# Performance work log

Hardware: AMD Instinct MI355X
Metric: run time of the kernel (lower is better)

The kernel has to match this reference:

```python
import jax, jax.numpy as jnp
import numpy as np

B, T = 32, 2048
HID, ACT, SRC, AGE = 512, 64, 2, 16
TRUNK, BINS, PHASES = 256, 20, 7
IN_DIM = HID + ACT + SRC + AGE  # 594


def setup_inputs() -> dict:
    key = jax.random.key(0)
    ks = jax.random.split(key, 16)
    s_in = 1.0 / np.sqrt(IN_DIM)
    s_tr = 1.0 / np.sqrt(TRUNK)
    s_h = 1.0 / np.sqrt(HID)
    return {
        "h_t": jax.random.normal(ks[0], (B, T, HID), jnp.float32),
        "a_t": jax.random.normal(ks[1], (B, T, ACT), jnp.float32),
        "d_t": jax.random.normal(ks[2], (B, T, SRC), jnp.float32),
        "age_embed": jax.random.normal(ks[3], (B, T, AGE), jnp.float32),
        "trunk_w": jax.random.normal(ks[4], (IN_DIM, TRUNK), jnp.float32) * s_in,
        "trunk_b": jax.random.normal(ks[5], (TRUNK,), jnp.float32) * s_in,
        "inst_base_w": jax.random.normal(ks[6], (TRUNK, BINS), jnp.float32) * s_tr,
        "inst_base_b": jax.random.normal(ks[7], (BINS,), jnp.float32) * s_tr,
        "group_base_w": jax.random.normal(ks[8], (TRUNK, BINS), jnp.float32) * s_tr,
        "group_base_b": jax.random.normal(ks[9], (BINS,), jnp.float32) * s_tr,
        "inst_exp_w": jax.random.normal(ks[10], (PHASES, TRUNK, BINS), jnp.float32) * s_tr,
        "inst_exp_b": jax.random.normal(ks[11], (PHASES, BINS), jnp.float32) * s_tr,
        "group_exp_w": jax.random.normal(ks[12], (PHASES, TRUNK, BINS), jnp.float32) * s_tr,
        "group_exp_b": jax.random.normal(ks[13], (PHASES, BINS), jnp.float32) * s_tr,
        "router_w": jax.random.normal(ks[14], (HID, PHASES), jnp.float32) * s_h,
        "router_b": jax.random.normal(ks[15], (PHASES,), jnp.float32) * s_h,
    }


def reference(h_t, a_t, d_t, age_embed,
              trunk_w, trunk_b, inst_base_w, inst_base_b,
              group_base_w, group_base_b, inst_exp_w, inst_exp_b,
              group_exp_w, group_exp_b, router_w, router_b):
    # Shared trunk: Linear(594,256) -> exact GELU
    x = jnp.concatenate([h_t, a_t, d_t, age_embed], axis=-1)  # [B,T,594]
    z = jax.nn.gelu(jnp.einsum('bti,io->bto', x, trunk_w) + trunk_b,
                    approximate=False)  # [B,T,256]

    # Soft phase routing from h_t
    pw = jax.nn.softmax(jnp.einsum('bth,hp->btp', h_t, router_w) + router_b,
                        axis=-1)  # [B,T,7]

    # Base heads
    inst_base = jnp.einsum('btd,dk->btk', z, inst_base_w) + inst_base_b
    group_base = jnp.einsum('btd,dk->btk', z, group_base_w) + group_base_b

    # All 7 experts as one batched GEMM, then weighted reduction over phases
    inst_e = jnp.einsum('btd,pdk->btpk', z, inst_exp_w) + inst_exp_b  # [B,T,7,20]
    group_e = jnp.einsum('btd,pdk->btpk', z, group_exp_w) + group_exp_b
    inst_res = jnp.einsum('btp,btpk->btk', pw, inst_e)
    group_res = jnp.einsum('btp,btpk->btk', pw, group_e)

    return (inst_base + inst_res, group_base + group_res)
```

## Files before the change

### kernel.cpp

```cpp
#include <hip/hip_runtime.h>
#include <math.h>

typedef unsigned int uint;
typedef unsigned short ushort;

using short8 = __attribute__((ext_vector_type(8))) short;
using f32x4  = __attribute__((ext_vector_type(4))) float;

#define BT      65536
#define HID     512
#define IN_DIM  594
#define TRUNK   256
#define BINS    20
#define NCOMBO  320

#define WT_P_SZ (19*16*64*8)
#define RP_SZ   (16*64*8)
#define WA_P_SZ (8*20*64*8)

__device__ inline ushort f2bf(float f) {
    uint u = __float_as_uint(f);
    return (ushort)((u + 0x7fffu + ((u >> 16) & 1u)) >> 16);
}

__global__ __launch_bounds__(64) void pack_all(
    const float* __restrict__ trunk_w, const float* __restrict__ router_w,
    const float* __restrict__ inst_base_w, const float* __restrict__ inst_base_b,
    const float* __restrict__ group_base_w, const float* __restrict__ group_base_b,
    const float* __restrict__ inst_exp_w, const float* __restrict__ inst_exp_b,
    const float* __restrict__ group_exp_w, const float* __restrict__ group_exp_b,
    ushort* __restrict__ WtP, ushort* __restrict__ RP,
    ushort* __restrict__ WaP, float* __restrict__ wbias)
{
    const int b = blockIdx.x, l = threadIdx.x;
    const int lr = l & 15, lg = l >> 4;
    if (b < 304) {
        int kk = b >> 4, n = b & 15;
        int col = n * 16 + lr;
        ushort* dst = WtP + ((size_t)(kk * 16 + n) * 64 + l) * 8;
        #pragma unroll
        for (int j = 0; j < 8; ++j) {
            int k = kk * 32 + lg * 8 + j;
            dst[j] = (k < IN_DIM) ? f2bf(trunk_w[k * TRUNK + col]) : (ushort)0;
        }
    } else if (b < 320) {
        int kk = b - 304;
        ushort* dst = RP + ((size_t)(kk * 64 + l)) * 8;
        #pragma unroll
        for (int j = 0; j < 8; ++j) {
            int k = kk * 32 + lg * 8 + j;
            dst[j] = (lr < 7) ? f2bf(router_w[k * 7 + lr]) : (ushort)0;
        }
    } else if (b < 480) {
        int b2 = b - 320, kk = b2 / 20, n = b2 % 20;
        int combo = n * 16 + lr;
        int h = combo / 160, rem = combo % 160, kb = rem >> 3, p = rem & 7;
        const float* bw = h ? group_base_w : inst_base_w;
        const float* ew = h ? group_exp_w  : inst_exp_w;
        ushort* dst = WaP + ((size_t)(kk * 20 + n) * 64 + l) * 8;
        #pragma unroll
        for (int j = 0; j < 8; ++j) {
            int k = kk * 32 + lg * 8 + j;
            float v = (p == 0) ? bw[k * BINS + kb]
                               : ew[((p - 1) * TRUNK + k) * BINS + kb];
            dst[j] = f2bf(v);
        }
    } else {
        for (int c = l; c < NCOMBO; c += 64) {
            int h = c / 160, rem = c % 160, kb = rem >> 3, p = rem & 7;
            const float* bb = h ? group_base_b : inst_base_b;
            const float* eb = h ? group_exp_b  : inst_exp_b;
            wbias[c] = (p == 0) ? bb[kb] : eb[(p - 1) * BINS + kb];
        }
    }
}

__global__ __launch_bounds__(256, 3) void fused_mfma(
    const float* __restrict__ h_t, const float* __restrict__ a_t,
    const float* __restrict__ d_t, const float* __restrict__ age,
    const float* __restrict__ trunk_b, const float* __restrict__ router_b,
    const ushort* __restrict__ WtP, const ushort* __restrict__ RP,
    const ushort* __restrict__ WaP, const float* __restrict__ wbias,
    float* __restrict__ out)
{
    __shared__ alignas(16) ushort zs[16384];

    const int tid = threadIdx.x;
    const int l = tid & 63, w = tid >> 6;
    const int lr = l & 15, lg = l >> 4;
    const int block0 = blockIdx.x * 64;

    const int srow = tid >> 2;
    const int sq   = tid & 3;
    const size_t stok = block0 + srow;

    ushort* xs = zs;

    f32x4 acc[4][4];
    f32x4 accr[4];
    #pragma unroll
    for (int mm = 0; mm < 4; ++mm) {
        accr[mm] = (f32x4){0.f,0.f,0.f,0.f};
        #pragma unroll
        for (int nn = 0; nn < 4; ++nn) acc[mm][nn] = (f32x4){0.f,0.f,0.f,0.f};
    }

    auto stage_load = [&](int kk, float4 ld[2]) {
        if (kk < 16) {
            const float4* p = (const float4*)(h_t + stok * HID + kk * 32 + sq * 8);
            ld[0] = p[0]; ld[1] = p[1];
        } else if (kk < 18) {
            const float4* p = (const float4*)(a_t + stok * 64 + (kk - 16) * 32 + sq * 8);
            ld[0] = p[0]; ld[1] = p[1];
        } else {
            float* f = (float*)ld;
            #pragma unroll
            for (int j = 0; j < 8; ++j) {
                int c = 576 + sq * 8 + j;
                float v;
                if (c < 578)      v = d_t[stok * 2 + (c - 576)];
                else if (c < 594) v = age[stok * 16 + (c - 578)];
                else              v = 0.f;
                f[j] = v;
            }
        }
    };
    auto stage_write = [&](int buf, float4 ld[2]) {
        const float* f = (const float*)ld;
        short8 v;
        #pragma unroll
        for (int j = 0; j < 8; ++j) v[j] = (short)f2bf(f[j]);
        *(short8*)(xs + buf * 2048 + ((srow >> 4) * 64 + (srow & 15) + sq * 16) * 8) = v;
    };

    {
        float4 ld[2];
        stage_load(0, ld);
        stage_write(0, ld);
        __syncthreads();
        int cur = 0;
        #pragma unroll 1
        for (int kk = 0; kk < 19; ++kk) {
            float4 nld[2];
            if (kk < 18) stage_load(kk + 1, nld);

            const ushort* xb = xs + cur * 2048;
            short8 a0 = *(const short8*)(xb + (0 * 64 + l) * 8);
            short8 a1 = *(const short8*)(xb + (1 * 64 + l) * 8);
            short8 a2 = *(const short8*)(xb + (2 * 64 + l) * 8);
            short8 a3 = *(const short8*)(xb + (3 * 64 + l) * 8);

            const ushort* wp = WtP + ((size_t)kk * 16 + w * 4) * 512;
            short8 bq[4];
            #pragma unroll
            for (int nn = 0; nn < 4; ++nn)
                bq[nn] = *(const short8*)(wp + (size_t)nn * 512 + l * 8);

            if (kk < 16) {
                short8 rb = *(const short8*)(RP + (size_t)kk * 512 + l * 8);
                accr[0] = __builtin_amdgcn_mfma_f32_16x16x32_bf16(a0, rb, accr[0],0,0,0);
                accr[1] = __builtin_amdgcn_mfma_f32_16x16x32_bf16(a1, rb, accr[1],0,0,0);
                accr[2] = __builtin_amdgcn_mfma_f32_16x16x32_bf16(a2, rb, accr[2],0,0,0);
                accr[3] = __builtin_amdgcn_mfma_f32_16x16x32_bf16(a3, rb, accr[3],0,0,0);
            }
            #pragma unroll
            for (int nn = 0; nn < 4; ++nn) {
                acc[0][nn] = __builtin_amdgcn_mfma_f32_16x16x32_bf16(a0, bq[nn], acc[0][nn],0,0,0);
                acc[1][nn] = __builtin_amdgcn_mfma_f32_16x16x32_bf16(a1, bq[nn], acc[1][nn],0,0,0);
                acc[2][nn] = __builtin_amdgcn_mfma_f32_16x16x32_bf16(a2, bq[nn], acc[2][nn],0,0,0);
                acc[3][nn] = __builtin_amdgcn_mfma_f32_16x16x32_bf16(a3, bq[nn], acc[3][nn],0,0,0);
            }

            if (kk < 18) stage_write(cur ^ 1, nld);
            __syncthreads();
            cur ^= 1;
        }
    }

    float pwv[4][4];
    {
        const float rb_l = (lr < 7) ? router_b[lr] : 0.f;
        #pragma unroll
        for (int mm = 0; mm < 4; ++mm)
        #pragma unroll
        for (int r = 0; r < 4; ++r) {
            float x = (lr < 7) ? (accr[mm][r] + rb_l) : -3.0e38f;
            float mx = x;
            mx = fmaxf(mx, __shfl_xor(mx, 1));
            mx = fmaxf(mx, __shfl_xor(mx, 2));
            mx = fmaxf(mx, __shfl_xor(mx, 4));
            mx = fmaxf(mx, __shfl_xor(mx, 8));
            float e = expf(x - mx);
            float s = e;
            s += __shfl_xor(s, 1);
            s += __shfl_xor(s, 2);
            s += __shfl_xor(s, 4);
            s += __shfl_xor(s, 8);
            pwv[mm][r] = e / s;
        }
    }

    {
        char* zb = (char*)zs;
        #pragma unroll
        for (int nn = 0; nn < 4; ++nn) {
            int colbase = (w * 4 + nn) * 16 + lr;
            float tb = trunk_b[colbase];
            #pragma unroll
            for (int mm = 0; mm < 4; ++mm)
            #pragma unroll
            for (int r = 0; r < 4; ++r) {
                float v = acc[mm][nn][r] + tb;
                v = 0.5f * v * (1.f + erff(v * 0.70710678118654752f));
                int row  = mm * 16 + lg * 4 + r;
                int slot = (colbase >> 3) ^ (row & 7);
                *(ushort*)(zb + row * 512 + slot * 16 + (colbase & 7) * 2) = f2bf(v);
            }
        }
    }
    __syncthreads();

    const char* zb = (const char*)zs;
    const int p8 = l & 7;
    const int csrc = (l & 48) | (p8 ? (p8 - 1) : 0);

    f32x4 acc2[4][5];
    #pragma unroll
    for (int mm = 0; mm < 4; ++mm)
    #pragma unroll
    for (int nn = 0; nn < 5; ++nn) acc2[mm][nn] = (f32x4){0.f,0.f,0.f,0.f};

    #pragma unroll
    for (int kk = 0; kk < 8; ++kk) {
        short8 a[4];
        #pragma unroll
        for (int mm = 0; mm < 4; ++mm) {
            int row = mm * 16 + lr;
            a[mm] = *(const short8*)(zb + row * 512 + (((kk * 4 + lg) ^ (row & 7)) << 4));
        }
        const ushort* wp = WaP + ((size_t)kk * 20 + w * 5) * 512;
        #pragma unroll
        for (int nn = 0; nn < 5; ++nn) {
            short8 bq = *(const short8*)(wp + (size_t)nn * 512 + l * 8);
            acc2[0][nn] = __builtin_amdgcn_mfma_f32_16x16x32_bf16(a[0], bq, acc2[0][nn],0,0,0);
            acc2[1][nn] = __builtin_amdgcn_mfma_f32_16x16x32_bf16(a[1], bq, acc2[1][nn],0,0,0);
            acc2[2][nn] = __builtin_amdgcn_mfma_f32_16x16x32_bf16(a[2], bq, acc2[2][nn],0,0,0);
            acc2[3][nn] = __builtin_amdgcn_mfma_f32_16x16x32_bf16(a[3], bq, acc2[3][nn],0,0,0);
        }
    }

    {
        float cw[4][4];
        #pragma unroll
        for (int mm = 0; mm < 4; ++mm)
        #pragma unroll
        for (int r = 0; r < 4; ++r)
            cw[mm][r] = __shfl(pwv[mm][r], csrc);

        #pragma unroll
        for (int nn = 0; nn < 5; ++nn) {
            int combo = (w * 5 + nn) * 16 + lr;
            float wb = wbias[combo];
            #pragma unroll
            for (int mm = 0; mm < 4; ++mm)
            #pragma unroll
            for (int r = 0; r < 4; ++r) {
                float e = acc2[mm][nn][r] + wb;
                float val = (p8 ? cw[mm][r] : 1.0f) * e;
                val += __shfl_xor(val, 1);
                val += __shfl_xor(val, 2);
                val += __shfl_xor(val, 4);
                if (p8 == 0) {
                    int h = combo / 160, rem = combo % 160, kb = rem >> 3;
                    size_t t = block0 + mm * 16 + lg * 4 + r;
                    out[(size_t)h * (BT * BINS) + t * BINS + kb] = val;
                }
            }
        }
    }
}

extern "C" void kernel_launch(void* const* d_in, const int* in_sizes, int n_in,
                              void* d_out, int out_size, void* d_ws, size_t ws_size,
                              hipStream_t stream) {
    const float* h_t          = (const float*)d_in[0];
    const float* a_t          = (const float*)d_in[1];
    const float* d_t          = (const float*)d_in[2];
    const float* age_embed    = (const float*)d_in[3];
    const float* trunk_w      = (const float*)d_in[4];
    const float* trunk_b      = (const float*)d_in[5];
    const float* inst_base_w  = (const float*)d_in[6];
    const float* inst_base_b  = (const float*)d_in[7];
    const float* group_base_w = (const float*)d_in[8];
    const float* group_base_b = (const float*)d_in[9];
    const float* inst_exp_w   = (const float*)d_in[10];
    const float* inst_exp_b   = (const float*)d_in[11];
    const float* group_exp_w  = (const float*)d_in[12];
    const float* group_exp_b  = (const float*)d_in[13];
    const float* router_w     = (const float*)d_in[14];
    const float* router_b     = (const float*)d_in[15];

    ushort* WtP   = (ushort*)d_ws;
    ushort* RP    = WtP + WT_P_SZ;
    ushort* WaP   = RP + RP_SZ;
    float*  wbias = (float*)(WaP + WA_P_SZ);

    pack_all<<<481, 64, 0, stream>>>(
        trunk_w, router_w,
        inst_base_w, inst_base_b, group_base_w, group_base_b,
        inst_exp_w, inst_exp_b, group_exp_w, group_exp_b,
        WtP, RP, WaP, wbias);

    fused_mfma<<<BT / 64, 256, 0, stream>>>(
        h_t, a_t, d_t, age_embed, trunk_b, router_b,
        WtP, RP, WaP, wbias, (float*)d_out);
}
```

Baseline: 110.9 us.

## Double block tile to 128 tokens, process two K-chunks per barrier, split router work

New measurement: 103.0 us. 1.08x faster.

```diff
diff --git a/kernel.cpp b/kernel.cpp
--- a/kernel.cpp
+++ b/kernel.cpp
@@ -75,7 +75,7 @@
     }
 }
 
-__global__ __launch_bounds__(256, 3) void fused_mfma(
+__global__ __launch_bounds__(256, 2) void fused_mfma(
     const float* __restrict__ h_t, const float* __restrict__ a_t,
     const float* __restrict__ d_t, const float* __restrict__ age,
     const float* __restrict__ trunk_b, const float* __restrict__ router_b,
@@ -83,40 +83,40 @@
     const ushort* __restrict__ WaP, const float* __restrict__ wbias,
     float* __restrict__ out)
 {
-    __shared__ alignas(16) ushort zs[16384];
+    __shared__ alignas(16) ushort zs[32768];
+    __shared__ float pwl[128 * 9];
 
     const int tid = threadIdx.x;
     const int l = tid & 63, w = tid >> 6;
     const int lr = l & 15, lg = l >> 4;
-    const int block0 = blockIdx.x * 64;
-
-    const int srow = tid >> 2;
-    const int sq   = tid & 3;
+    const int block0 = blockIdx.x * 128;
+
+    const int srow = tid >> 1;
+    const int half = tid & 1;
     const size_t stok = block0 + srow;
 
     ushort* xs = zs;
 
-    f32x4 acc[4][4];
-    f32x4 accr[4];
-    #pragma unroll
-    for (int mm = 0; mm < 4; ++mm) {
-        accr[mm] = (f32x4){0.f,0.f,0.f,0.f};
-        #pragma unroll
-        for (int nn = 0; nn < 4; ++nn) acc[mm][nn] = (f32x4){0.f,0.f,0.f,0.f};
-    }
-
-    auto stage_load = [&](int kk, float4 ld[2]) {
+    f32x4 acc[8][4];
+    f32x4 accr0 = (f32x4){0.f,0.f,0.f,0.f};
+    f32x4 accr1 = (f32x4){0.f,0.f,0.f,0.f};
+    #pragma unroll
+    for (int mm = 0; mm < 8; ++mm)
+    #pragma unroll
+    for (int nn = 0; nn < 4; ++nn) acc[mm][nn] = (f32x4){0.f,0.f,0.f,0.f};
+
+    auto stage_load_one = [&](int kk, float4* dst) {
         if (kk < 16) {
-            const float4* p = (const float4*)(h_t + stok * HID + kk * 32 + sq * 8);
-            ld[0] = p[0]; ld[1] = p[1];
+            const float4* p = (const float4*)(h_t + stok * HID + kk * 32 + half * 16);
+            dst[0]=p[0]; dst[1]=p[1]; dst[2]=p[2]; dst[3]=p[3];
         } else if (kk < 18) {
-            const float4* p = (const float4*)(a_t + stok * 64 + (kk - 16) * 32 + sq * 8);
-            ld[0] = p[0]; ld[1] = p[1];
+            const float4* p = (const float4*)(a_t + stok * 64 + (kk - 16) * 32 + half * 16);
+            dst[0]=p[0]; dst[1]=p[1]; dst[2]=p[2]; dst[3]=p[3];
         } else {
-            float* f = (float*)ld;
-            #pragma unroll
-            for (int j = 0; j < 8; ++j) {
-                int c = 576 + sq * 8 + j;
+            float* f = (float*)dst;
+            #pragma unroll
+            for (int j = 0; j < 16; ++j) {
+                int c = 576 + half * 16 + j;
                 float v;
                 if (c < 578)      v = d_t[stok * 2 + (c - 576)];
                 else if (c < 594) v = age[stok * 16 + (c - 578)];
@@ -125,66 +125,90 @@
             }
         }
     };
-    auto stage_write = [&](int buf, float4 ld[2]) {
+    auto stage_write_one = [&](int buf, int slot, const float4* ld) {
         const float* f = (const float*)ld;
-        short8 v;
-        #pragma unroll
-        for (int j = 0; j < 8; ++j) v[j] = (short)f2bf(f[j]);
-        *(short8*)(xs + buf * 2048 + ((srow >> 4) * 64 + (srow & 15) + sq * 16) * 8) = v;
+        short8 v0, v1;
+        #pragma unroll
+        for (int j = 0; j < 8; ++j) {
+            v0[j] = (short)f2bf(f[j]);
+            v1[j] = (short)f2bf(f[j + 8]);
+        }
+        ushort* dst = xs + buf * 8192 + slot * 4096
+                      + (srow >> 4) * 512 + ((srow & 15) + half * 32) * 8;
+        *(short8*)dst = v0;
+        *(short8*)(dst + 128) = v1;
     };
 
+    auto mfma_chunk = [&](const ushort* xb, int kk, bool do_router) {
+        short8 a[8];
+        #pragma unroll
+        for (int mm = 0; mm < 8; ++mm)
+            a[mm] = *(const short8*)(xb + (mm * 64 + l) * 8);
+        if (do_router) {
+            short8 rb  = *(const short8*)(RP + (size_t)kk * 512 + l * 8);
+            short8 ar0 = *(const short8*)(xb + ((2 * w + 0) * 64 + l) * 8);
+            short8 ar1 = *(const short8*)(xb + ((2 * w + 1) * 64 + l) * 8);
+            accr0 = __builtin_amdgcn_mfma_f32_16x16x32_bf16(ar0, rb, accr0, 0, 0, 0);
+            accr1 = __builtin_amdgcn_mfma_f32_16x16x32_bf16(ar1, rb, accr1, 0, 0, 0);
+        }
+        const ushort* wp = WtP + ((size_t)kk * 16 + w * 4) * 512;
+        #pragma unroll
+        for (int nn = 0; nn < 4; ++nn) {
+            short8 bq = *(const short8*)(wp + (size_t)nn * 512 + l * 8);
+            acc[0][nn] = __builtin_amdgcn_mfma_f32_16x16x32_bf16(a[0], bq, acc[0][nn],0,0,0);
+            acc[1][nn] = __builtin_amdgcn_mfma_f32_16x16x32_bf16(a[1], bq, acc[1][nn],0,0,0);
+            acc[2][nn] = __builtin_amdgcn_mfma_f32_16x16x32_bf16(a[2], bq, acc[2][nn],0,0,0);
+            acc[3][nn] = __builtin_amdgcn_mfma_f32_16x16x32_bf16(a[3], bq, acc[3][nn],0,0,0);
+            acc[4][nn] = __builtin_amdgcn_mfma_f32_16x16x32_bf16(a[4], bq, acc[4][nn],0,0,0);
+            acc[5][nn] = __builtin_amdgcn_mfma_f32_16x16x32_bf16(a[5], bq, acc[5][nn],0,0,0);
+            acc[6][nn] = __builtin_amdgcn_mfma_f32_16x16x32_bf16(a[6], bq, acc[6][nn],0,0,0);
+            acc[7][nn] = __builtin_amdgcn_mfma_f32_16x16x32_bf16(a[7], bq, acc[7][nn],0,0,0);
+        }
+    };
+
     {
-        float4 ld[2];
-        stage_load(0, ld);
-        stage_write(0, ld);
+        float4 ld[8];
+        stage_load_one(0, ld);
+        stage_load_one(1, ld + 4);
+        stage_write_one(0, 0, ld);
+        stage_write_one(0, 1, ld + 4);
         __syncthreads();
         int cur = 0;
         #pragma unroll 1
-        for (int kk = 0; kk < 19; ++kk) {
-            float4 nld[2];
-            if (kk < 18) stage_load(kk + 1, nld);
-
-            const ushort* xb = xs + cur * 2048;
-            short8 a0 = *(const short8*)(xb + (0 * 64 + l) * 8);
-            short8 a1 = *(const short8*)(xb + (1 * 64 + l) * 8);
-            short8 a2 = *(const short8*)(xb + (2 * 64 + l) * 8);
-            short8 a3 = *(const short8*)(xb + (3 * 64 + l) * 8);
-
-            const ushort* wp = WtP + ((size_t)kk * 16 + w * 4) * 512;
-            short8 bq[4];
-            #pragma unroll
-            for (int nn = 0; nn < 4; ++nn)
-                bq[nn] = *(const short8*)(wp + (size_t)nn * 512 + l * 8);
-
-            if (kk < 16) {
-                short8 rb = *(const short8*)(RP + (size_t)kk * 512 + l * 8);
-                accr[0] = __builtin_amdgcn_mfma_f32_16x16x32_bf16(a0, rb, accr[0],0,0,0);
-                accr[1] = __builtin_amdgcn_mfma_f32_16x16x32_bf16(a1, rb, accr[1],0,0,0);
-                accr[2] = __builtin_amdgcn_mfma_f32_16x16x32_bf16(a2, rb, accr[2],0,0,0);
-                accr[3] = __builtin_amdgcn_mfma_f32_16x16x32_bf16(a3, rb, accr[3],0,0,0);
-            }
-            #pragma unroll
-            for (int nn = 0; nn < 4; ++nn) {
-                acc[0][nn] = __builtin_amdgcn_mfma_f32_16x16x32_bf16(a0, bq[nn], acc[0][nn],0,0,0);
-                acc[1][nn] = __builtin_amdgcn_mfma_f32_16x16x32_bf16(a1, bq[nn], acc[1][nn],0,0,0);
-                acc[2][nn] = __builtin_amdgcn_mfma_f32_16x16x32_bf16(a2, bq[nn], acc[2][nn],0,0,0);
-                acc[3][nn] = __builtin_amdgcn_mfma_f32_16x16x32_bf16(a3, bq[nn], acc[3][nn],0,0,0);
-            }
-
-            if (kk < 18) stage_write(cur ^ 1, nld);
+        for (int i = 0; i < 8; ++i) {
+            float4 nld[8];
+            stage_load_one(2 * i + 2, nld);
+            stage_load_one(2 * i + 3, nld + 4);
+            const ushort* xb = xs + cur * 8192;
+            mfma_chunk(xb,        2 * i,     true);
+            mfma_chunk(xb + 4096, 2 * i + 1, true);
+            stage_write_one(cur ^ 1, 0, nld);
+            stage_write_one(cur ^ 1, 1, nld + 4);
             __syncthreads();
             cur ^= 1;
         }
-    }
-
-    float pwv[4][4];
+        {
+            float4 tld[4];
+            stage_load_one(18, tld);
+            const ushort* xb = xs + cur * 8192;
+            mfma_chunk(xb,        16, false);
+            mfma_chunk(xb + 4096, 17, false);
+            stage_write_one(cur ^ 1, 0, tld);
+            __syncthreads();
+            cur ^= 1;
+        }
+        mfma_chunk(xs + cur * 8192, 18, false);
+    }
+
     {
         const float rb_l = (lr < 7) ? router_b[lr] : 0.f;
-        #pragma unroll
-        for (int mm = 0; mm < 4; ++mm)
+        float pwv[2][4];
+        #pragma unroll
+        for (int m = 0; m < 2; ++m)
         #pragma unroll
         for (int r = 0; r < 4; ++r) {
-            float x = (lr < 7) ? (accr[mm][r] + rb_l) : -3.0e38f;
+            float lv = (m == 0) ? accr0[r] : accr1[r];
+            float x = (lr < 7) ? (lv + rb_l) : -3.0e38f;
             float mx = x;
             mx = fmaxf(mx, __shfl_xor(mx, 1));
             mx = fmaxf(mx, __shfl_xor(mx, 2));
@@ -196,7 +220,14 @@
             s += __shfl_xor(s, 2);
             s += __shfl_xor(s, 4);
             s += __shfl_xor(s, 8);
-            pwv[mm][r] = e / s;
+            pwv[m][r] = e / s;
+        }
+        if (lr < 7) {
+            #pragma unroll
+            for (int m = 0; m < 2; ++m)
+            #pragma unroll
+            for (int r = 0; r < 4; ++r)
+                pwl[(w * 32 + m * 16 + lg * 4 + r) * 9 + lr] = pwv[m][r];
         }
     }
 
@@ -207,7 +238,7 @@
             int colbase = (w * 4 + nn) * 16 + lr;
             float tb = trunk_b[colbase];
             #pragma unroll
-            for (int mm = 0; mm < 4; ++mm)
+            for (int mm = 0; mm < 8; ++mm)
             #pragma unroll
             for (int r = 0; r < 4; ++r) {
                 float v = acc[mm][nn][r] + tb;
@@ -222,19 +253,18 @@
 
     const char* zb = (const char*)zs;
     const int p8 = l & 7;
-    const int csrc = (l & 48) | (p8 ? (p8 - 1) : 0);
-
-    f32x4 acc2[4][5];
-    #pragma unroll
-    for (int mm = 0; mm < 4; ++mm)
+
+    f32x4 acc2[8][5];
+    #pragma unroll
+    for (int mm = 0; mm < 8; ++mm)
     #pragma unroll
     for (int nn = 0; nn < 5; ++nn) acc2[mm][nn] = (f32x4){0.f,0.f,0.f,0.f};
 
     #pragma unroll
     for (int kk = 0; kk < 8; ++kk) {
-        short8 a[4];
-        #pragma unroll
-        for (int mm = 0; mm < 4; ++mm) {
+        short8 a[8];
+        #pragma unroll
+        for (int mm = 0; mm < 8; ++mm) {
             int row = mm * 16 + lr;
             a[mm] = *(const short8*)(zb + row * 512 + (((kk * 4 + lg) ^ (row & 7)) << 4));
         }
@@ -246,32 +276,37 @@
             acc2[1][nn] = __builtin_amdgcn_mfma_f32_16x16x32_bf16(a[1], bq, acc2[1][nn],0,0,0);
             acc2[2][nn] = __builtin_amdgcn_mfma_f32_16x16x32_bf16(a[2], bq, acc2[2][nn],0,0,0);
             acc2[3][nn] = __builtin_amdgcn_mfma_f32_16x16x32_bf16(a[3], bq, acc2[3][nn],0,0,0);
+            acc2[4][nn] = __builtin_amdgcn_mfma_f32_16x16x32_bf16(a[4], bq, acc2[4][nn],0,0,0);
+            acc2[5][nn] = __builtin_amdgcn_mfma_f32_16x16x32_bf16(a[5], bq, acc2[5][nn],0,0,0);
+            acc2[6][nn] = __builtin_amdgcn_mfma_f32_16x16x32_bf16(a[6], bq, acc2[6][nn],0,0,0);
+            acc2[7][nn] = __builtin_amdgcn_mfma_f32_16x16x32_bf16(a[7], bq, acc2[7][nn],0,0,0);
         }
     }
 
     {
-        float cw[4][4];
-        #pragma unroll
-        for (int mm = 0; mm < 4; ++mm)
+        float cwv[8][4];
+        const int psel = p8 ? (p8 - 1) : 0;
+        #pragma unroll
+        for (int mm = 0; mm < 8; ++mm)
         #pragma unroll
         for (int r = 0; r < 4; ++r)
-            cw[mm][r] = __shfl(pwv[mm][r], csrc);
+            cwv[mm][r] = pwl[(mm * 16 + lg * 4 + r) * 9 + psel];
 
         #pragma unroll
         for (int nn = 0; nn < 5; ++nn) {
             int combo = (w * 5 + nn) * 16 + lr;
             float wb = wbias[combo];
-            #pragma unroll
-            for (int mm = 0; mm < 4; ++mm)
+            int h = combo / 160, rem = combo % 160, kb = rem >> 3;
+            #pragma unroll
+            for (int mm = 0; mm < 8; ++mm)
             #pragma unroll
             for (int r = 0; r < 4; ++r) {
                 float e = acc2[mm][nn][r] + wb;
-                float val = (p8 ? cw[mm][r] : 1.0f) * e;
+                float val = (p8 ? cwv[mm][r] : 1.0f) * e;
                 val += __shfl_xor(val, 1);
                 val += __shfl_xor(val, 2);
                 val += __shfl_xor(val, 4);
                 if (p8 == 0) {
-                    int h = combo / 160, rem = combo % 160, kb = rem >> 3;
                     size_t t = block0 + mm * 16 + lg * 4 + r;
                     out[(size_t)h * (BT * BINS) + t * BINS + kb] = val;
                 }
@@ -311,7 +346,7 @@
         inst_exp_w, inst_exp_b, group_exp_w, group_exp_b,
         WtP, RP, WaP, wbias);
 
-    fused_mfma<<<BT / 64, 256, 0, stream>>>(
+    fused_mfma<<<BT / 128, 256, 0, stream>>>(
         h_t, a_t, d_t, age_embed, trunk_b, router_b,
         WtP, RP, WaP, wbias, (float*)d_out);
 }
```

## Load trunk A-operand directly from global into MFMA registers, drop LDS staging

Applied to the files above, without the earlier changes.

Result: slower. 182.5 us (+64.5%).

```diff
diff --git a/kernel.cpp b/kernel.cpp
--- a/kernel.cpp
+++ b/kernel.cpp
@@ -1,4 +1,5 @@
 #include <hip/hip_runtime.h>
+#include <hip/hip_bf16.h>
 #include <math.h>
 
 typedef unsigned int uint;
@@ -21,6 +22,20 @@
 __device__ inline ushort f2bf(float f) {
     uint u = __float_as_uint(f);
     return (ushort)((u + 0x7fffu + ((u >> 16) & 1u)) >> 16);
+}
+
+__device__ inline uint pk2(float lo, float hi) {
+    union { __hip_bfloat162 b; uint u; } cv;
+    cv.b = __float22bfloat162_rn(float2{lo, hi});
+    return cv.u;
+}
+__device__ inline short8 cvt8pk(float4 a, float4 b) {
+    union { uint4 t; short8 s; } cv;
+    cv.t.x = pk2(a.x, a.y);
+    cv.t.y = pk2(a.z, a.w);
+    cv.t.z = pk2(b.x, b.y);
+    cv.t.w = pk2(b.z, b.w);
+    return cv.s;
 }
 
 __global__ __launch_bounds__(64) void pack_all(
@@ -75,7 +90,7 @@
     }
 }
 
-__global__ __launch_bounds__(256, 3) void fused_mfma(
+__global__ __launch_bounds__(256, 2) void fused_mfma(
     const float* __restrict__ h_t, const float* __restrict__ a_t,
     const float* __restrict__ d_t, const float* __restrict__ age,
     const float* __restrict__ trunk_b, const float* __restrict__ router_b,
@@ -83,19 +98,13 @@
     const ushort* __restrict__ WaP, const float* __restrict__ wbias,
     float* __restrict__ out)
 {
-    __shared__ alignas(16) ushort zs[16384];
+    __shared__ alignas(16) ushort zs[64 * 256];
 
     const int tid = threadIdx.x;
     const int l = tid & 63, w = tid >> 6;
     const int lr = l & 15, lg = l >> 4;
     const int block0 = blockIdx.x * 64;
 
-    const int srow = tid >> 2;
-    const int sq   = tid & 3;
-    const size_t stok = block0 + srow;
-
-    ushort* xs = zs;
-
     f32x4 acc[4][4];
     f32x4 accr[4];
     #pragma unroll
@@ -105,75 +114,74 @@
         for (int nn = 0; nn < 4; ++nn) acc[mm][nn] = (f32x4){0.f,0.f,0.f,0.f};
     }
 
-    auto stage_load = [&](int kk, float4 ld[2]) {
-        if (kk < 16) {
-            const float4* p = (const float4*)(h_t + stok * HID + kk * 32 + sq * 8);
-            ld[0] = p[0]; ld[1] = p[1];
-        } else if (kk < 18) {
-            const float4* p = (const float4*)(a_t + stok * 64 + (kk - 16) * 32 + sq * 8);
-            ld[0] = p[0]; ld[1] = p[1];
-        } else {
-            float* f = (float*)ld;
+    #pragma unroll 2
+    for (int kk = 0; kk < 16; ++kk) {
+        short8 a[4];
+        #pragma unroll
+        for (int mm = 0; mm < 4; ++mm) {
+            const float4* p = (const float4*)(h_t
+                + (size_t)(block0 + mm * 16 + lr) * HID + kk * 32 + lg * 8);
+            a[mm] = cvt8pk(p[0], p[1]);
+        }
+        short8 rb = *(const short8*)(RP + (size_t)kk * 512 + l * 8);
+        accr[0] = __builtin_amdgcn_mfma_f32_16x16x32_bf16(a[0], rb, accr[0],0,0,0);
+        accr[1] = __builtin_amdgcn_mfma_f32_16x16x32_bf16(a[1], rb, accr[1],0,0,0);
+        accr[2] = __builtin_amdgcn_mfma_f32_16x16x32_bf16(a[2], rb, accr[2],0,0,0);
+        accr[3] = __builtin_amdgcn_mfma_f32_16x16x32_bf16(a[3], rb, accr[3],0,0,0);
+        const ushort* wp = WtP + ((size_t)kk * 16 + w * 4) * 512;
+        #pragma unroll
+        for (int nn = 0; nn < 4; ++nn) {
+            short8 bq = *(const short8*)(wp + (size_t)nn * 512 + l * 8);
+            acc[0][nn] = __builtin_amdgcn_mfma_f32_16x16x32_bf16(a[0], bq, acc[0][nn],0,0,0);
+            acc[1][nn] = __builtin_amdgcn_mfma_f32_16x16x32_bf16(a[1], bq, acc[1][nn],0,0,0);
+            acc[2][nn] = __builtin_amdgcn_mfma_f32_16x16x32_bf16(a[2], bq, acc[2][nn],0,0,0);
+            acc[3][nn] = __builtin_amdgcn_mfma_f32_16x16x32_bf16(a[3], bq, acc[3][nn],0,0,0);
+        }
+    }
+    #pragma unroll
+    for (int kk = 16; kk < 18; ++kk) {
+        short8 a[4];
+        #pragma unroll
+        for (int mm = 0; mm < 4; ++mm) {
+            const float4* p = (const float4*)(a_t
+                + (size_t)(block0 + mm * 16 + lr) * 64 + (kk - 16) * 32 + lg * 8);
+            a[mm] = cvt8pk(p[0], p[1]);
+        }
+        const ushort* wp = WtP + ((size_t)kk * 16 + w * 4) * 512;
+        #pragma unroll
+        for (int nn = 0; nn < 4; ++nn) {
+            short8 bq = *(const short8*)(wp + (size_t)nn * 512 + l * 8);
+            acc[0][nn] = __builtin_amdgcn_mfma_f32_16x16x32_bf16(a[0], bq, acc[0][nn],0,0,0);
+            acc[1][nn] = __builtin_amdgcn_mfma_f32_16x16x32_bf16(a[1], bq, acc[1][nn],0,0,0);
+            acc[2][nn] = __builtin_amdgcn_mfma_f32_16x16x32_bf16(a[2], bq, acc[2][nn],0,0,0);
+            acc[3][nn] = __builtin_amdgcn_mfma_f32_16x16x32_bf16(a[3], bq, acc[3][nn],0,0,0);
+        }
+    }
+    {
+        short8 a[4];
+        #pragma unroll
+        for (int mm = 0; mm < 4; ++mm) {
+            size_t tok = block0 + mm * 16 + lr;
+            float f[8];
             #pragma unroll
             for (int j = 0; j < 8; ++j) {
-                int c = 576 + sq * 8 + j;
+                int c = 576 + lg * 8 + j;
                 float v;
-                if (c < 578)      v = d_t[stok * 2 + (c - 576)];
-                else if (c < 594) v = age[stok * 16 + (c - 578)];
+                if (c < 578)      v = d_t[tok * 2 + (c - 576)];
+                else if (c < 594) v = age[tok * 16 + (c - 578)];
                 else              v = 0.f;
                 f[j] = v;
             }
-        }
-    };
-    auto stage_write = [&](int buf, float4 ld[2]) {
-        const float* f = (const float*)ld;
-        short8 v;
-        #pragma unroll
-        for (int j = 0; j < 8; ++j) v[j] = (short)f2bf(f[j]);
-        *(short8*)(xs + buf * 2048 + ((srow >> 4) * 64 + (srow & 15) + sq * 16) * 8) = v;
-    };
-
-    {
-        float4 ld[2];
-        stage_load(0, ld);
-        stage_write(0, ld);
-        __syncthreads();
-        int cur = 0;
-        #pragma unroll 1
-        for (int kk = 0; kk < 19; ++kk) {
-            float4 nld[2];
-            if (kk < 18) stage_load(kk + 1, nld);
-
-            const ushort* xb = xs + cur * 2048;
-            short8 a0 = *(const short8*)(xb + (0 * 64 + l) * 8);
-            short8 a1 = *(const short8*)(xb + (1 * 64 + l) * 8);
-            short8 a2 = *(const short8*)(xb + (2 * 64 + l) * 8);
-            short8 a3 = *(const short8*)(xb + (3 * 64 + l) * 8);
-
-            const ushort* wp = WtP + ((size_t)kk * 16 + w * 4) * 512;
-            short8 bq[4];
-            #pragma unroll
-            for (int nn = 0; nn < 4; ++nn)
-                bq[nn] = *(const short8*)(wp + (size_t)nn * 512 + l * 8);
-
-            if (kk < 16) {
-                short8 rb = *(const short8*)(RP + (size_t)kk * 512 + l * 8);
-                accr[0] = __builtin_amdgcn_mfma_f32_16x16x32_bf16(a0, rb, accr[0],0,0,0);
-                accr[1] = __builtin_amdgcn_mfma_f32_16x16x32_bf16(a1, rb, accr[1],0,0,0);
-                accr[2] = __builtin_amdgcn_mfma_f32_16x16x32_bf16(a2, rb, accr[2],0,0,0);
-                accr[3] = __builtin_amdgcn_mfma_f32_16x16x32_bf16(a3, rb, accr[3],0,0,0);
-            }
-            #pragma unroll
-            for (int nn = 0; nn < 4; ++nn) {
-                acc[0][nn] = __builtin_amdgcn_mfma_f32_16x16x32_bf16(a0, bq[nn], acc[0][nn],0,0,0);
-                acc[1][nn] = __builtin_amdgcn_mfma_f32_16x16x32_bf16(a1, bq[nn], acc[1][nn],0,0,0);
-                acc[2][nn] = __builtin_amdgcn_mfma_f32_16x16x32_bf16(a2, bq[nn], acc[2][nn],0,0,0);
-                acc[3][nn] = __builtin_amdgcn_mfma_f32_16x16x32_bf16(a3, bq[nn], acc[3][nn],0,0,0);
-            }
-
-            if (kk < 18) stage_write(cur ^ 1, nld);
-            __syncthreads();
-            cur ^= 1;
+            a[mm] = cvt8pk(float4{f[0],f[1],f[2],f[3]}, float4{f[4],f[5],f[6],f[7]});
+        }
+        const ushort* wp = WtP + ((size_t)18 * 16 + w * 4) * 512;
+        #pragma unroll
+        for (int nn = 0; nn < 4; ++nn) {
+            short8 bq = *(const short8*)(wp + (size_t)nn * 512 + l * 8);
+            acc[0][nn] = __builtin_amdgcn_mfma_f32_16x16x32_bf16(a[0], bq, acc[0][nn],0,0,0);
+            acc[1][nn] = __builtin_amdgcn_mfma_f32_16x16x32_bf16(a[1], bq, acc[1][nn],0,0,0);
+            acc[2][nn] = __builtin_amdgcn_mfma_f32_16x16x32_bf16(a[2], bq, acc[2][nn],0,0,0);
+            acc[3][nn] = __builtin_amdgcn_mfma_f32_16x16x32_bf16(a[3], bq, acc[3][nn],0,0,0);
         }
     }
 
@@ -261,6 +269,7 @@
         for (int nn = 0; nn < 5; ++nn) {
             int combo = (w * 5 + nn) * 16 + lr;
             float wb = wbias[combo];
+            int h = combo / 160, rem = combo % 160, kb = rem >> 3;
             #pragma unroll
             for (int mm = 0; mm < 4; ++mm)
             #pragma unroll
@@ -271,7 +280,6 @@
                 val += __shfl_xor(val, 2);
                 val += __shfl_xor(val, 4);
                 if (p8 == 0) {
-                    int h = combo / 160, rem = combo % 160, kb = rem >> 3;
                     size_t t = block0 + mm * 16 + lg * 4 + r;
                     out[(size_t)h * (BT * BINS) + t * BINS + kb] = val;
                 }
```
